# Kernel optimization log

Hardware: AMD Instinct MI355X
Metric: run time of the kernel (lower is better)

The kernel has to match this reference:

```python
import jax, jax.numpy as jnp
import numpy as np

HIDDEN = 4096
N_HEADS = 32
N_KV_HEADS = 8
HEAD_DIM = 128
MAX_POS = 4096
N_GROUPS = N_HEADS // N_KV_HEADS  # 4


def _sincos_table():
    # create_sinusoidal_positions(MAX_POS, HEAD_DIM) -> [MAX_POS, 1, 2*HEAD_DIM]
    inv_freq = 1.0 / 10000 ** (np.arange(0, HEAD_DIM, 2) / HEAD_DIM)
    freqs = np.einsum('i,j->ij', np.arange(MAX_POS), inv_freq).astype('float32')
    emb = np.concatenate((freqs, freqs), axis=-1)  # [MAX_POS, HEAD_DIM]
    out = np.concatenate((np.sin(emb)[:, None, :], np.cos(emb)[:, None, :]), axis=-1)
    return jnp.asarray(out[:, :, :MAX_POS])  # slice is a no-op since 2*HEAD_DIM < MAX_POS

_SINCOS = _sincos_table()


def _rotate_half(t):
    half = t.shape[-1] // 2
    return jnp.concatenate((-t[..., half:], t[..., :half]), axis=-1)


def setup_inputs() -> dict:
    key = jax.random.key(0)
    ks = jax.random.split(key, 9)
    B, S = 1, 2048
    scale = 0.02
    return {
        'hidden_states': jax.random.normal(ks[0], (B, S, HIDDEN), jnp.float32),
        'attention_mask': jnp.ones((B, 1, 1, S), jnp.bool_),
        'position_ids': jnp.broadcast_to(jnp.arange(S, dtype=jnp.int32)[None, :], (B, S)),
        'Wq': jax.random.normal(ks[1], (HIDDEN, N_HEADS * HEAD_DIM), jnp.float32) * scale,
        'bq': jnp.zeros((N_HEADS * HEAD_DIM,), jnp.float32),
        'Wk': jax.random.normal(ks[2], (HIDDEN, N_KV_HEADS * HEAD_DIM), jnp.float32) * scale,
        'bk': jnp.zeros((N_KV_HEADS * HEAD_DIM,), jnp.float32),
        'Wv': jax.random.normal(ks[3], (HIDDEN, N_KV_HEADS * HEAD_DIM), jnp.float32) * scale,
        'bv': jnp.zeros((N_KV_HEADS * HEAD_DIM,), jnp.float32),
        'Wo': jax.random.normal(ks[4], (N_HEADS * HEAD_DIM, HIDDEN), jnp.float32) * scale,
        'bo': jnp.zeros((HIDDEN,), jnp.float32),
    }


def reference(hidden_states, attention_mask, position_ids, Wq, bq, Wk, bk, Wv, bv, Wo, bo):
    B, S, _ = hidden_states.shape
    # QKV projections + split heads
    q = (hidden_states @ Wq + bq).reshape(B, S, N_HEADS, HEAD_DIM)
    k = (hidden_states @ Wk + bk).reshape(B, S, N_KV_HEADS, HEAD_DIM)
    v = (hidden_states @ Wv + bv).reshape(B, S, N_KV_HEADS, HEAD_DIM)
    # Rotary embedding: sincos[position_ids] -> [B,S,1,2*HEAD_DIM]
    sincos = _SINCOS[position_ids]
    sin_pos, cos_pos = jnp.split(sincos, 2, axis=-1)  # each [B,S,1,HEAD_DIM]
    k = k * cos_pos + _rotate_half(k) * sin_pos
    q = q * cos_pos + _rotate_half(q) * sin_pos
    # Causal mask combined with padding mask
    causal = jnp.tril(jnp.ones((S, S), jnp.bool_))[None, None]  # [1,1,S,S]
    mask = jnp.logical_and(attention_mask, causal)  # [B,1,S,S]
    # GQA: repeat kv heads
    k = jnp.repeat(k, N_GROUPS, axis=2)  # [B,S,H,D]
    v = jnp.repeat(v, N_GROUPS, axis=2)
    bias = jnp.where(mask, 0.0, jnp.finfo(jnp.float32).min).astype(jnp.float32)
    scores = jnp.einsum('bqhd,bkhd->bhqk', q, k) / jnp.sqrt(jnp.float32(HEAD_DIM)) + bias
    attn_weights = jax.nn.softmax(scores, axis=-1)  # [B,H,S,S]
    attn_output = jnp.einsum('bhqk,bkhd->bqhd', attn_weights, v).reshape(B, S, N_HEADS * HEAD_DIM)
    return attn_output @ Wo + bo
```

## Files before the change

### kernel.cpp

```cpp
#include <hip/hip_runtime.h>
#include <hip/hip_bf16.h>
#include <math.h>

typedef __bf16 bf16x8 __attribute__((ext_vector_type(8)));
typedef __bf16 bf16x4 __attribute__((ext_vector_type(4)));
typedef float  f32x4  __attribute__((ext_vector_type(4)));
typedef unsigned int u32;

#define S_LEN 2048
#define HID   4096
#define NH    32
#define NKV   8
#define HD    128

__device__ inline void gld_lds16(const __bf16* g, __bf16* l) {
  __builtin_amdgcn_global_load_lds((const __attribute__((address_space(1))) u32*)g,
                                   (__attribute__((address_space(3))) u32*)l,
                                   16, 0, 0);
}

__global__ void cast_bf16(const float* __restrict__ in, __bf16* __restrict__ out, int n4) {
  int i = blockIdx.x * blockDim.x + threadIdx.x;
  if (i < n4) {
    float4 v = ((const float4*)in)[i];
    bf16x4 o;
    o[0] = (__bf16)v.x; o[1] = (__bf16)v.y; o[2] = (__bf16)v.z; o[3] = (__bf16)v.w;
    ((bf16x4*)out)[i] = o;
  }
}

template <typename T>
__global__ void transpose_cast(const T* __restrict__ in, __bf16* __restrict__ out,
                               int ldi, int ldo) {
  __shared__ float tile[32][33];
  const int c0 = blockIdx.x * 32, r0 = blockIdx.y * 32;
  const int tx = threadIdx.x, ty = threadIdx.y;
  for (int j = 0; j < 32; j += 8)
    tile[ty + j][tx] = (float)in[(size_t)(r0 + ty + j) * ldi + c0 + tx];
  __syncthreads();
  for (int j = 0; j < 32; j += 8)
    out[(size_t)(c0 + ty + j) * ldo + r0 + tx] = (__bf16)tile[tx][ty + j];
}

__global__ void concat_bias(const float* __restrict__ bk, const float* __restrict__ bv,
                            float* __restrict__ out) {
  int i = blockIdx.x * blockDim.x + threadIdx.x;
  if (i < 2048) out[i] = (i < 1024) ? bk[i] : bv[i - 1024];
}

template <typename CT>
__global__ __launch_bounds__(256) void gemm_bt(const __bf16* __restrict__ A,
                                               const __bf16* __restrict__ Bt,
                                               const float* __restrict__ bias,
                                               CT* __restrict__ C,
                                               int M, int N, int K) {
  __shared__ __bf16 As[128 * 64];
  __shared__ __bf16 Bs[128 * 64];
  const int tid  = threadIdx.x;
  const int lane = tid & 63;
  const int lrow = lane & 15, quad = lane >> 4;
  const int wave = tid >> 6;
  const int wm = (wave & 1) * 64, wn = (wave >> 1) * 64;
  const int m0 = blockIdx.y * 128, n0 = blockIdx.x * 128;

  f32x4 acc[4][4] = {};

  const __bf16* aP[4];
  const __bf16* bP[4];
  __bf16* aL[4];
  __bf16* bL[4];
#pragma unroll
  for (int s = 0; s < 4; s++) {
    const int c = tid + 256 * s;
    const int row = c >> 3;
    const int kc = ((c & 7) + row) & 7;
    aP[s] = A + (size_t)(m0 + row) * K + kc * 8;
    bP[s] = Bt + (size_t)(n0 + row) * K + kc * 8;
    aL[s] = As + c * 8;
    bL[s] = Bs + c * 8;
  }

  int offA[2][4], offB[2][4];
#pragma unroll
  for (int h = 0; h < 2; h++)
#pragma unroll
    for (int t = 0; t < 4; t++) {
      const int ra = wm + t * 16 + lrow;
      const int rb = wn + t * 16 + lrow;
      offA[h][t] = (ra * 8 + ((h * 4 + quad - ra) & 7)) * 8;
      offB[h][t] = (rb * 8 + ((h * 4 + quad - rb) & 7)) * 8;
    }

  for (int k0 = 0; k0 < K; k0 += 64) {
    __syncthreads();
#pragma unroll
    for (int s = 0; s < 4; s++) {
      gld_lds16(aP[s] + k0, aL[s]);
      gld_lds16(bP[s] + k0, bL[s]);
    }
    __syncthreads();

#pragma unroll
    for (int h = 0; h < 2; h++) {
      bf16x8 af[4], bfr[4];
#pragma unroll
      for (int t = 0; t < 4; t++) {
        af[t]  = *(const bf16x8*)(As + offA[h][t]);
        bfr[t] = *(const bf16x8*)(Bs + offB[h][t]);
      }
#pragma unroll
      for (int i = 0; i < 4; i++)
#pragma unroll
        for (int j = 0; j < 4; j++)
          acc[i][j] = __builtin_amdgcn_mfma_f32_16x16x32_bf16(af[i], bfr[j], acc[i][j], 0, 0, 0);
    }
  }

#pragma unroll
  for (int i = 0; i < 4; i++) {
    const int row = m0 + wm + i * 16 + quad * 4;
#pragma unroll
    for (int j = 0; j < 4; j++) {
      const int col = n0 + wn + j * 16 + lrow;
      const float b = bias[col];
#pragma unroll
      for (int r = 0; r < 4; r++)
        C[(size_t)(row + r) * N + col] = (CT)(acc[i][j][r] + b);
    }
  }
}

__global__ void rope_inplace(__bf16* __restrict__ Q, __bf16* __restrict__ KV,
                             const int* __restrict__ pos_ids) {
  const int s = blockIdx.y;
  const int t = blockIdx.x * blockDim.x + threadIdx.x;
  const int h = t >> 6, j = t & 63;
  const float pos = (float)pos_ids[s];
  const float inv_freq = __builtin_exp2f((float)j * -0.2076205059304601f);
  const float ang = pos * inv_freq;
  float sn, cs;
  sincosf(ang, &sn, &cs);
  if (h < NH) {
    __bf16* p = Q + (size_t)s * HID + h * HD + j;
    const float x0 = (float)p[0], x1 = (float)p[64];
    p[0]  = (__bf16)(x0 * cs - x1 * sn);
    p[64] = (__bf16)(x1 * cs + x0 * sn);
  } else {
    const int hk = h - NH;
    __bf16* p = KV + (size_t)s * 2048 + hk * HD + j;
    const float x0 = (float)p[0], x1 = (float)p[64];
    p[0]  = (__bf16)(x0 * cs - x1 * sn);
    p[64] = (__bf16)(x1 * cs + x0 * sn);
  }
}

__global__ __launch_bounds__(256) void flash_attn(const __bf16* __restrict__ Qb,
                                                  const __bf16* __restrict__ Kb,
                                                  const __bf16* __restrict__ Vt,
                                                  __bf16* __restrict__ attn, int ldk) {
  __shared__ __bf16 Ks[2][32 * 128];
  __shared__ __bf16 Vs[2][128 * 32];
  __shared__ __bf16 Plds[4][2][16][40];
  const int tid  = threadIdx.x;
  const int wave = tid >> 6;
  const int lane = tid & 63;
  const int lrow = lane & 15, quad = lane >> 4;

  const int c = blockIdx.x & 255, p = blockIdx.x >> 8;
  const int h = c >> 3;
  const int xh = c & 7;
  const int xx = p ? xh : 15 - xh;
  const int bq0 = xx * 128;
  const int kvh = h >> 2;
  const int T0 = bq0 + wave * 16;
  const int T1 = T0 + 64;
  const int kend = bq0 + 128;

  const __bf16* kg[2];
  const __bf16* vg[2];
  __bf16* kL[2];
  __bf16* vL[2];
#pragma unroll
  for (int s = 0; s < 2; s++) {
    const int ck = tid + 256 * s;
    const int key = ck >> 4, kcb = ((ck & 15) + key) & 15;
    kg[s] = Kb + (size_t)key * ldk + kvh * HD + kcb * 8;
    kL[s] = (__bf16*)0 + ck * 8;
    const int cv = tid + 256 * s;
    const int d = cv >> 2, vcb = ((cv & 3) + d) & 3;
    vg[s] = Vt + (size_t)(kvh * HD + d) * S_LEN + vcb * 8;
    vL[s] = (__bf16*)0 + cv * 8;
  }

  int offK0[4], offK1[4], offV[8];
#pragma unroll
  for (int kc = 0; kc < 4; kc++) {
    const int rot = (kc * 4 + quad - lrow) & 15;
    offK0[kc] = (lrow * 16 + rot) * 8;
    offK1[kc] = ((lrow + 16) * 16 + rot) * 8;
  }
#pragma unroll
  for (int dt = 0; dt < 8; dt++) {
    const int d = dt * 16 + lrow;
    offV[dt] = (d * 4 + ((quad - d) & 3)) * 8;
  }

  bf16x8 qf[2][4];
#pragma unroll
  for (int m = 0; m < 2; m++) {
    const __bf16* qbase = Qb + (size_t)(T0 + m * 64 + lrow) * HID + h * HD + quad * 8;
#pragma unroll
    for (int kc = 0; kc < 4; kc++) qf[m][kc] = *(const bf16x8*)(qbase + kc * 32);
  }

  f32x4 o[2][8] = {};
  f32x4 lac[2] = {};
  bf16x8 ones;
#pragma unroll
  for (int j = 0; j < 8; j++) ones[j] = (__bf16)1.0f;

  const float cs = 0.08838834764831845f * 1.44269504088896f;

#pragma unroll
  for (int s = 0; s < 2; s++) {
    gld_lds16(kg[s], &Ks[0][0] + (size_t)(kL[s] - (__bf16*)0));
    gld_lds16(vg[s], &Vs[0][0] + (size_t)(vL[s] - (__bf16*)0));
  }

  int cur = 0;
  for (int kb = 0; kb < kend; kb += 32) {
    __syncthreads();
    if (kb + 32 < kend) {
      const int nxt = cur ^ 1;
#pragma unroll
      for (int s = 0; s < 2; s++) {
        gld_lds16(kg[s] + (size_t)(kb + 32) * ldk, &Ks[nxt][0] + (size_t)(kL[s] - (__bf16*)0));
        gld_lds16(vg[s] + (kb + 32), &Vs[nxt][0] + (size_t)(vL[s] - (__bf16*)0));
      }
    }

    bf16x8 kf0[4], kf1[4];
#pragma unroll
    for (int kc = 0; kc < 4; kc++) {
      kf0[kc] = *(const bf16x8*)(&Ks[cur][offK0[kc]]);
      kf1[kc] = *(const bf16x8*)(&Ks[cur][offK1[kc]]);
    }
    f32x4 s[2][2] = {};
#pragma unroll
    for (int kc = 0; kc < 4; kc++) {
      s[0][0] = __builtin_amdgcn_mfma_f32_16x16x32_bf16(qf[0][kc], kf0[kc], s[0][0], 0, 0, 0);
      s[0][1] = __builtin_amdgcn_mfma_f32_16x16x32_bf16(qf[0][kc], kf1[kc], s[0][1], 0, 0, 0);
      s[1][0] = __builtin_amdgcn_mfma_f32_16x16x32_bf16(qf[1][kc], kf0[kc], s[1][0], 0, 0, 0);
      s[1][1] = __builtin_amdgcn_mfma_f32_16x16x32_bf16(qf[1][kc], kf1[kc], s[1][1], 0, 0, 0);
    }
#pragma unroll
    for (int m = 0; m < 2; m++) {
      const int Tm = m ? T1 : T0;
#pragma unroll
      for (int n = 0; n < 2; n++) {
        const int col = kb + n * 16 + lrow;
#pragma unroll
        for (int r = 0; r < 4; r++) {
          const int row = Tm + quad * 4 + r;
          const float pv = (col <= row) ? __builtin_exp2f(s[m][n][r] * cs) : 0.0f;
          Plds[wave][m][quad * 4 + r][n * 16 + lrow] = (__bf16)pv;
        }
      }
    }
    bf16x8 pf0 = *(const bf16x8*)(&Plds[wave][0][lrow][quad * 8]);
    bf16x8 pf1 = *(const bf16x8*)(&Plds[wave][1][lrow][quad * 8]);
#pragma unroll
    for (int dt = 0; dt < 8; dt++) {
      bf16x8 vf = *(const bf16x8*)(&Vs[cur][offV[dt]]);
      o[0][dt] = __builtin_amdgcn_mfma_f32_16x16x32_bf16(pf0, vf, o[0][dt], 0, 0, 0);
      o[1][dt] = __builtin_amdgcn_mfma_f32_16x16x32_bf16(pf1, vf, o[1][dt], 0, 0, 0);
    }
    lac[0] = __builtin_amdgcn_mfma_f32_16x16x32_bf16(pf0, ones, lac[0], 0, 0, 0);
    lac[1] = __builtin_amdgcn_mfma_f32_16x16x32_bf16(pf1, ones, lac[1], 0, 0, 0);
    cur ^= 1;
  }

#pragma unroll
  for (int m = 0; m < 2; m++) {
    const int Tm = m ? T1 : T0;
#pragma unroll
    for (int r = 0; r < 4; r++) {
      const float inv_l = 1.0f / lac[m][r];
      const size_t rowoff = (size_t)(Tm + quad * 4 + r) * HID + h * HD;
#pragma unroll
      for (int dt = 0; dt < 8; dt++)
        attn[rowoff + dt * 16 + lrow] = (__bf16)(o[m][dt][r] * inv_l);
    }
  }
}

extern "C" void kernel_launch(void* const* d_in, const int* in_sizes, int n_in,
                              void* d_out, int out_size, void* d_ws, size_t ws_size,
                              hipStream_t stream) {
  const float* hs = (const float*)d_in[0];
  const int* pos = (const int*)d_in[2];
  const float* Wq = (const float*)d_in[3];
  const float* bq = (const float*)d_in[4];
  const float* Wk = (const float*)d_in[5];
  const float* bk = (const float*)d_in[6];
  const float* Wv = (const float*)d_in[7];
  const float* bv = (const float*)d_in[8];
  const float* Wo = (const float*)d_in[9];
  const float* bo = (const float*)d_in[10];
  float* out = (float*)d_out;
  char* ws = (char*)d_ws;
  char* oc = (char*)d_out;

  __bf16* bHS   = (__bf16*)(ws + 0);
  __bf16* bWT   = (__bf16*)(ws + ((size_t)16 << 20));
  __bf16* bAttn = bHS;
  __bf16* bQ   = (__bf16*)(oc + 0);
  __bf16* bKV  = (__bf16*)(oc + ((size_t)16 << 20));
  __bf16* bVt  = (__bf16*)(oc + ((size_t)24 << 20));
  float*  bKVb = (float*)(oc + ((size_t)28 << 20));

  dim3 tb(32, 8);

  cast_bf16<<<8192, 256, 0, stream>>>(hs, bHS, (S_LEN * HID) / 4);
  transpose_cast<float><<<dim3(128, 128), tb, 0, stream>>>(Wq, bWT, 4096, 4096);
  gemm_bt<__bf16><<<dim3(32, 16), 256, 0, stream>>>(bHS, bWT, bq, bQ, 2048, 4096, 4096);
  transpose_cast<float><<<dim3(32, 128), tb, 0, stream>>>(Wk, bWT, 1024, 4096);
  transpose_cast<float><<<dim3(32, 128), tb, 0, stream>>>(Wv, bWT + (size_t)1024 * 4096, 1024, 4096);
  concat_bias<<<8, 256, 0, stream>>>(bk, bv, bKVb);
  gemm_bt<__bf16><<<dim3(16, 16), 256, 0, stream>>>(bHS, bWT, bKVb, bKV, 2048, 2048, 4096);
  rope_inplace<<<dim3(10, 2048), 256, 0, stream>>>(bQ, bKV, pos);
  transpose_cast<__bf16><<<dim3(32, 64), tb, 0, stream>>>(bKV + 1024, bVt, 2048, 2048);
  flash_attn<<<512, 256, 0, stream>>>(bQ, bKV, bVt, bAttn, 2048);
  transpose_cast<float><<<dim3(128, 128), tb, 0, stream>>>(Wo, bWT, 4096, 4096);
  gemm_bt<float><<<dim3(32, 16), 256, 0, stream>>>(bAttn, bWT, bo, out, 2048, 4096, 4096);
}
```

Before: 567.9 us.

## Use 2-wave flash attention blocks with 64 query rows per wave and causal skipping

Flash attention now runs with 128 threads (2 waves) per block instead of 4, and each wave owns 64 contiguous query rows. Each K/V fragment read from LDS is therefore reused across four row tiles instead of two. Waves skip key blocks lying entirely above their causal diagonal, and tiles fully below the diagonal drop the per-element mask test. The costs are more registers per wave, fewer waves per block to hide latency, more loads per thread, and an adjusted V LDS swizzle.

```diff
diff --git a/kernel.cpp b/kernel.cpp
--- a/kernel.cpp
+++ b/kernel.cpp
@@ -154,13 +154,13 @@
   }
 }
 
-__global__ __launch_bounds__(256) void flash_attn(const __bf16* __restrict__ Qb,
-                                                  const __bf16* __restrict__ Kb,
-                                                  const __bf16* __restrict__ Vt,
-                                                  __bf16* __restrict__ attn, int ldk) {
+__global__ __launch_bounds__(128, 1) void flash_attn(const __bf16* __restrict__ Qb,
+                                                     const __bf16* __restrict__ Kb,
+                                                     const __bf16* __restrict__ Vt,
+                                                     __bf16* __restrict__ attn, int ldk) {
   __shared__ __bf16 Ks[2][32 * 128];
   __shared__ __bf16 Vs[2][128 * 32];
-  __shared__ __bf16 Plds[4][2][16][40];
+  __shared__ __bf16 Plds[2][4][16][40];
   const int tid  = threadIdx.x;
   const int wave = tid >> 6;
   const int lane = tid & 63;
@@ -172,24 +172,21 @@
   const int xx = p ? xh : 15 - xh;
   const int bq0 = xx * 128;
   const int kvh = h >> 2;
-  const int T0 = bq0 + wave * 16;
-  const int T1 = T0 + 64;
+  const int Tw = bq0 + wave * 64;
   const int kend = bq0 + 128;
 
-  const __bf16* kg[2];
-  const __bf16* vg[2];
-  __bf16* kL[2];
-  __bf16* vL[2];
-#pragma unroll
-  for (int s = 0; s < 2; s++) {
-    const int ck = tid + 256 * s;
+  const __bf16* kg[4];
+  const __bf16* vg[4];
+  int kL[4], vL[4];
+#pragma unroll
+  for (int s = 0; s < 4; s++) {
+    const int ck = tid + 128 * s;
     const int key = ck >> 4, kcb = ((ck & 15) + key) & 15;
     kg[s] = Kb + (size_t)key * ldk + kvh * HD + kcb * 8;
-    kL[s] = (__bf16*)0 + ck * 8;
-    const int cv = tid + 256 * s;
-    const int d = cv >> 2, vcb = ((cv & 3) + d) & 3;
+    kL[s] = ck * 8;
+    const int d = ck >> 2, vcb = ((ck & 3) - (d >> 1)) & 3;
     vg[s] = Vt + (size_t)(kvh * HD + d) * S_LEN + vcb * 8;
-    vL[s] = (__bf16*)0 + cv * 8;
+    vL[s] = ck * 8;
   }
 
   int offK0[4], offK1[4], offV[8];
@@ -202,19 +199,19 @@
 #pragma unroll
   for (int dt = 0; dt < 8; dt++) {
     const int d = dt * 16 + lrow;
-    offV[dt] = (d * 4 + ((quad - d) & 3)) * 8;
-  }
-
-  bf16x8 qf[2][4];
-#pragma unroll
-  for (int m = 0; m < 2; m++) {
-    const __bf16* qbase = Qb + (size_t)(T0 + m * 64 + lrow) * HID + h * HD + quad * 8;
+    offV[dt] = (d * 4 + ((quad + (d >> 1)) & 3)) * 8;
+  }
+
+  bf16x8 qf[4][4];
+#pragma unroll
+  for (int m = 0; m < 4; m++) {
+    const __bf16* qbase = Qb + (size_t)(Tw + m * 16 + lrow) * HID + h * HD + quad * 8;
 #pragma unroll
     for (int kc = 0; kc < 4; kc++) qf[m][kc] = *(const bf16x8*)(qbase + kc * 32);
   }
 
-  f32x4 o[2][8] = {};
-  f32x4 lac[2] = {};
+  f32x4 o[4][8] = {};
+  f32x4 lac[4] = {};
   bf16x8 ones;
 #pragma unroll
   for (int j = 0; j < 8; j++) ones[j] = (__bf16)1.0f;
@@ -222,9 +219,9 @@
   const float cs = 0.08838834764831845f * 1.44269504088896f;
 
 #pragma unroll
-  for (int s = 0; s < 2; s++) {
-    gld_lds16(kg[s], &Ks[0][0] + (size_t)(kL[s] - (__bf16*)0));
-    gld_lds16(vg[s], &Vs[0][0] + (size_t)(vL[s] - (__bf16*)0));
+  for (int s = 0; s < 4; s++) {
+    gld_lds16(kg[s], &Ks[0][0] + kL[s]);
+    gld_lds16(vg[s], &Vs[0][0] + vL[s]);
   }
 
   int cur = 0;
@@ -233,56 +230,71 @@
     if (kb + 32 < kend) {
       const int nxt = cur ^ 1;
 #pragma unroll
-      for (int s = 0; s < 2; s++) {
-        gld_lds16(kg[s] + (size_t)(kb + 32) * ldk, &Ks[nxt][0] + (size_t)(kL[s] - (__bf16*)0));
-        gld_lds16(vg[s] + (kb + 32), &Vs[nxt][0] + (size_t)(vL[s] - (__bf16*)0));
-      }
-    }
-
-    bf16x8 kf0[4], kf1[4];
-#pragma unroll
-    for (int kc = 0; kc < 4; kc++) {
-      kf0[kc] = *(const bf16x8*)(&Ks[cur][offK0[kc]]);
-      kf1[kc] = *(const bf16x8*)(&Ks[cur][offK1[kc]]);
-    }
-    f32x4 s[2][2] = {};
-#pragma unroll
-    for (int kc = 0; kc < 4; kc++) {
-      s[0][0] = __builtin_amdgcn_mfma_f32_16x16x32_bf16(qf[0][kc], kf0[kc], s[0][0], 0, 0, 0);
-      s[0][1] = __builtin_amdgcn_mfma_f32_16x16x32_bf16(qf[0][kc], kf1[kc], s[0][1], 0, 0, 0);
-      s[1][0] = __builtin_amdgcn_mfma_f32_16x16x32_bf16(qf[1][kc], kf0[kc], s[1][0], 0, 0, 0);
-      s[1][1] = __builtin_amdgcn_mfma_f32_16x16x32_bf16(qf[1][kc], kf1[kc], s[1][1], 0, 0, 0);
-    }
-#pragma unroll
-    for (int m = 0; m < 2; m++) {
-      const int Tm = m ? T1 : T0;
-#pragma unroll
-      for (int n = 0; n < 2; n++) {
-        const int col = kb + n * 16 + lrow;
-#pragma unroll
-        for (int r = 0; r < 4; r++) {
-          const int row = Tm + quad * 4 + r;
-          const float pv = (col <= row) ? __builtin_exp2f(s[m][n][r] * cs) : 0.0f;
-          Plds[wave][m][quad * 4 + r][n * 16 + lrow] = (__bf16)pv;
+      for (int s = 0; s < 4; s++) {
+        gld_lds16(kg[s] + (size_t)(kb + 32) * ldk, &Ks[nxt][0] + kL[s]);
+        gld_lds16(vg[s] + (kb + 32), &Vs[nxt][0] + vL[s]);
+      }
+    }
+
+    if (kb < Tw + 64) {
+      bf16x8 kf0[4], kf1[4];
+#pragma unroll
+      for (int kc = 0; kc < 4; kc++) {
+        kf0[kc] = *(const bf16x8*)(&Ks[cur][offK0[kc]]);
+        kf1[kc] = *(const bf16x8*)(&Ks[cur][offK1[kc]]);
+      }
+      f32x4 sc[4][2] = {};
+#pragma unroll
+      for (int kc = 0; kc < 4; kc++) {
+#pragma unroll
+        for (int m = 0; m < 4; m++) {
+          sc[m][0] = __builtin_amdgcn_mfma_f32_16x16x32_bf16(qf[m][kc], kf0[kc], sc[m][0], 0, 0, 0);
+          sc[m][1] = __builtin_amdgcn_mfma_f32_16x16x32_bf16(qf[m][kc], kf1[kc], sc[m][1], 0, 0, 0);
         }
       }
-    }
-    bf16x8 pf0 = *(const bf16x8*)(&Plds[wave][0][lrow][quad * 8]);
-    bf16x8 pf1 = *(const bf16x8*)(&Plds[wave][1][lrow][quad * 8]);
-#pragma unroll
-    for (int dt = 0; dt < 8; dt++) {
-      bf16x8 vf = *(const bf16x8*)(&Vs[cur][offV[dt]]);
-      o[0][dt] = __builtin_amdgcn_mfma_f32_16x16x32_bf16(pf0, vf, o[0][dt], 0, 0, 0);
-      o[1][dt] = __builtin_amdgcn_mfma_f32_16x16x32_bf16(pf1, vf, o[1][dt], 0, 0, 0);
-    }
-    lac[0] = __builtin_amdgcn_mfma_f32_16x16x32_bf16(pf0, ones, lac[0], 0, 0, 0);
-    lac[1] = __builtin_amdgcn_mfma_f32_16x16x32_bf16(pf1, ones, lac[1], 0, 0, 0);
+#pragma unroll
+      for (int m = 0; m < 4; m++) {
+        const int rmin = Tw + m * 16;
+        if (kb + 31 <= rmin) {
+#pragma unroll
+          for (int n = 0; n < 2; n++)
+#pragma unroll
+            for (int r = 0; r < 4; r++)
+              Plds[wave][m][quad * 4 + r][n * 16 + lrow] =
+                  (__bf16)__builtin_exp2f(sc[m][n][r] * cs);
+        } else {
+          const int rb = rmin + quad * 4;
+#pragma unroll
+          for (int n = 0; n < 2; n++) {
+            const int col = kb + n * 16 + lrow;
+#pragma unroll
+            for (int r = 0; r < 4; r++) {
+              const float pv = (col <= rb + r) ? __builtin_exp2f(sc[m][n][r] * cs) : 0.0f;
+              Plds[wave][m][quad * 4 + r][n * 16 + lrow] = (__bf16)pv;
+            }
+          }
+        }
+      }
+      bf16x8 pf[4];
+#pragma unroll
+      for (int m = 0; m < 4; m++) pf[m] = *(const bf16x8*)(&Plds[wave][m][lrow][quad * 8]);
+#pragma unroll
+      for (int dt = 0; dt < 8; dt++) {
+        bf16x8 vf = *(const bf16x8*)(&Vs[cur][offV[dt]]);
+#pragma unroll
+        for (int m = 0; m < 4; m++)
+          o[m][dt] = __builtin_amdgcn_mfma_f32_16x16x32_bf16(pf[m], vf, o[m][dt], 0, 0, 0);
+      }
+#pragma unroll
+      for (int m = 0; m < 4; m++)
+        lac[m] = __builtin_amdgcn_mfma_f32_16x16x32_bf16(pf[m], ones, lac[m], 0, 0, 0);
+    }
     cur ^= 1;
   }
 
 #pragma unroll
-  for (int m = 0; m < 2; m++) {
-    const int Tm = m ? T1 : T0;
+  for (int m = 0; m < 4; m++) {
+    const int Tm = Tw + m * 16;
 #pragma unroll
     for (int r = 0; r < 4; r++) {
       const float inv_l = 1.0f / lac[m][r];
@@ -330,7 +342,7 @@
   gemm_bt<__bf16><<<dim3(16, 16), 256, 0, stream>>>(bHS, bWT, bKVb, bKV, 2048, 2048, 4096);
   rope_inplace<<<dim3(10, 2048), 256, 0, stream>>>(bQ, bKV, pos);
   transpose_cast<__bf16><<<dim3(32, 64), tb, 0, stream>>>(bKV + 1024, bVt, 2048, 2048);
-  flash_attn<<<512, 256, 0, stream>>>(bQ, bKV, bVt, bAttn, 2048);
+  flash_attn<<<512, 128, 0, stream>>>(bQ, bKV, bVt, bAttn, 2048);
   transpose_cast<float><<<dim3(128, 128), tb, 0, stream>>>(Wo, bWT, 4096, 4096);
   gemm_bt<float><<<dim3(32, 16), 256, 0, stream>>>(bAttn, bWT, bo, out, 2048, 4096, 4096);
 }
```

Measured after the change: 621.7 us. 9.5% more time.

## Skip fully-masked causal tiles per wave, add unmasked fast path and swizzle fix

Applied to the files above, without the earlier changes.

Each wave now skips the QK^T and PV MFMAs for row groups whose rows all lie above the current key block, since those tiles are entirely masked. Tiles that are entirely below the diagonal skip the per-element causal compare. The V LDS swizzle changes to a new rotation, likely to cut bank conflicts on the transposed V reads, and s_setprio is raised around the MFMA bursts. The cost is added branching inside waves and a risk of imbalance across the block's waves, since the block barrier still forces them to step through every key block together.

```diff
diff --git a/kernel.cpp b/kernel.cpp
--- a/kernel.cpp
+++ b/kernel.cpp
@@ -178,18 +178,16 @@
 
   const __bf16* kg[2];
   const __bf16* vg[2];
-  __bf16* kL[2];
-  __bf16* vL[2];
+  int kL[2], vL[2];
 #pragma unroll
   for (int s = 0; s < 2; s++) {
     const int ck = tid + 256 * s;
     const int key = ck >> 4, kcb = ((ck & 15) + key) & 15;
     kg[s] = Kb + (size_t)key * ldk + kvh * HD + kcb * 8;
-    kL[s] = (__bf16*)0 + ck * 8;
-    const int cv = tid + 256 * s;
-    const int d = cv >> 2, vcb = ((cv & 3) + d) & 3;
+    kL[s] = ck * 8;
+    const int d = ck >> 2, vcb = ((ck & 3) - (d >> 1)) & 3;
     vg[s] = Vt + (size_t)(kvh * HD + d) * S_LEN + vcb * 8;
-    vL[s] = (__bf16*)0 + cv * 8;
+    vL[s] = ck * 8;
   }
 
   int offK0[4], offK1[4], offV[8];
@@ -202,7 +200,7 @@
 #pragma unroll
   for (int dt = 0; dt < 8; dt++) {
     const int d = dt * 16 + lrow;
-    offV[dt] = (d * 4 + ((quad - d) & 3)) * 8;
+    offV[dt] = (d * 4 + ((quad + (d >> 1)) & 3)) * 8;
   }
 
   bf16x8 qf[2][4];
@@ -223,8 +221,8 @@
 
 #pragma unroll
   for (int s = 0; s < 2; s++) {
-    gld_lds16(kg[s], &Ks[0][0] + (size_t)(kL[s] - (__bf16*)0));
-    gld_lds16(vg[s], &Vs[0][0] + (size_t)(vL[s] - (__bf16*)0));
+    gld_lds16(kg[s], &Ks[0][0] + kL[s]);
+    gld_lds16(vg[s], &Vs[0][0] + vL[s]);
   }
 
   int cur = 0;
@@ -234,49 +232,86 @@
       const int nxt = cur ^ 1;
 #pragma unroll
       for (int s = 0; s < 2; s++) {
-        gld_lds16(kg[s] + (size_t)(kb + 32) * ldk, &Ks[nxt][0] + (size_t)(kL[s] - (__bf16*)0));
-        gld_lds16(vg[s] + (kb + 32), &Vs[nxt][0] + (size_t)(vL[s] - (__bf16*)0));
-      }
-    }
-
-    bf16x8 kf0[4], kf1[4];
-#pragma unroll
-    for (int kc = 0; kc < 4; kc++) {
-      kf0[kc] = *(const bf16x8*)(&Ks[cur][offK0[kc]]);
-      kf1[kc] = *(const bf16x8*)(&Ks[cur][offK1[kc]]);
-    }
-    f32x4 s[2][2] = {};
-#pragma unroll
-    for (int kc = 0; kc < 4; kc++) {
-      s[0][0] = __builtin_amdgcn_mfma_f32_16x16x32_bf16(qf[0][kc], kf0[kc], s[0][0], 0, 0, 0);
-      s[0][1] = __builtin_amdgcn_mfma_f32_16x16x32_bf16(qf[0][kc], kf1[kc], s[0][1], 0, 0, 0);
-      s[1][0] = __builtin_amdgcn_mfma_f32_16x16x32_bf16(qf[1][kc], kf0[kc], s[1][0], 0, 0, 0);
-      s[1][1] = __builtin_amdgcn_mfma_f32_16x16x32_bf16(qf[1][kc], kf1[kc], s[1][1], 0, 0, 0);
-    }
-#pragma unroll
-    for (int m = 0; m < 2; m++) {
-      const int Tm = m ? T1 : T0;
-#pragma unroll
-      for (int n = 0; n < 2; n++) {
-        const int col = kb + n * 16 + lrow;
-#pragma unroll
-        for (int r = 0; r < 4; r++) {
-          const int row = Tm + quad * 4 + r;
-          const float pv = (col <= row) ? __builtin_exp2f(s[m][n][r] * cs) : 0.0f;
-          Plds[wave][m][quad * 4 + r][n * 16 + lrow] = (__bf16)pv;
-        }
-      }
-    }
-    bf16x8 pf0 = *(const bf16x8*)(&Plds[wave][0][lrow][quad * 8]);
-    bf16x8 pf1 = *(const bf16x8*)(&Plds[wave][1][lrow][quad * 8]);
-#pragma unroll
-    for (int dt = 0; dt < 8; dt++) {
-      bf16x8 vf = *(const bf16x8*)(&Vs[cur][offV[dt]]);
-      o[0][dt] = __builtin_amdgcn_mfma_f32_16x16x32_bf16(pf0, vf, o[0][dt], 0, 0, 0);
-      o[1][dt] = __builtin_amdgcn_mfma_f32_16x16x32_bf16(pf1, vf, o[1][dt], 0, 0, 0);
-    }
-    lac[0] = __builtin_amdgcn_mfma_f32_16x16x32_bf16(pf0, ones, lac[0], 0, 0, 0);
-    lac[1] = __builtin_amdgcn_mfma_f32_16x16x32_bf16(pf1, ones, lac[1], 0, 0, 0);
+        gld_lds16(kg[s] + (size_t)(kb + 32) * ldk, &Ks[nxt][0] + kL[s]);
+        gld_lds16(vg[s] + (kb + 32), &Vs[nxt][0] + vL[s]);
+      }
+    }
+
+    const bool live0 = (kb <= T0 + 15);
+    const bool live1 = (kb <= T1 + 15);
+
+    if (live1) {
+      bf16x8 kf0[4], kf1[4];
+#pragma unroll
+      for (int kc = 0; kc < 4; kc++) {
+        kf0[kc] = *(const bf16x8*)(&Ks[cur][offK0[kc]]);
+        kf1[kc] = *(const bf16x8*)(&Ks[cur][offK1[kc]]);
+      }
+      f32x4 sc[2][2] = {};
+      __builtin_amdgcn_s_setprio(1);
+      if (live0) {
+#pragma unroll
+        for (int kc = 0; kc < 4; kc++) {
+          sc[0][0] = __builtin_amdgcn_mfma_f32_16x16x32_bf16(qf[0][kc], kf0[kc], sc[0][0], 0, 0, 0);
+          sc[0][1] = __builtin_amdgcn_mfma_f32_16x16x32_bf16(qf[0][kc], kf1[kc], sc[0][1], 0, 0, 0);
+          sc[1][0] = __builtin_amdgcn_mfma_f32_16x16x32_bf16(qf[1][kc], kf0[kc], sc[1][0], 0, 0, 0);
+          sc[1][1] = __builtin_amdgcn_mfma_f32_16x16x32_bf16(qf[1][kc], kf1[kc], sc[1][1], 0, 0, 0);
+        }
+      } else {
+#pragma unroll
+        for (int kc = 0; kc < 4; kc++) {
+          sc[1][0] = __builtin_amdgcn_mfma_f32_16x16x32_bf16(qf[1][kc], kf0[kc], sc[1][0], 0, 0, 0);
+          sc[1][1] = __builtin_amdgcn_mfma_f32_16x16x32_bf16(qf[1][kc], kf1[kc], sc[1][1], 0, 0, 0);
+        }
+      }
+      __builtin_amdgcn_s_setprio(0);
+
+#pragma unroll
+      for (int m = 0; m < 2; m++) {
+        if (m == 0 && !live0) continue;
+        const int Tm = m ? T1 : T0;
+        if (kb + 31 <= Tm) {
+#pragma unroll
+          for (int n = 0; n < 2; n++)
+#pragma unroll
+            for (int r = 0; r < 4; r++)
+              Plds[wave][m][quad * 4 + r][n * 16 + lrow] =
+                  (__bf16)__builtin_exp2f(sc[m][n][r] * cs);
+        } else {
+          const int rb = Tm + quad * 4;
+#pragma unroll
+          for (int n = 0; n < 2; n++) {
+            const int col = kb + n * 16 + lrow;
+#pragma unroll
+            for (int r = 0; r < 4; r++) {
+              const float pv = (col <= rb + r) ? __builtin_exp2f(sc[m][n][r] * cs) : 0.0f;
+              Plds[wave][m][quad * 4 + r][n * 16 + lrow] = (__bf16)pv;
+            }
+          }
+        }
+      }
+      bf16x8 pf1 = *(const bf16x8*)(&Plds[wave][1][lrow][quad * 8]);
+      __builtin_amdgcn_s_setprio(1);
+      if (live0) {
+        bf16x8 pf0 = *(const bf16x8*)(&Plds[wave][0][lrow][quad * 8]);
+#pragma unroll
+        for (int dt = 0; dt < 8; dt++) {
+          bf16x8 vf = *(const bf16x8*)(&Vs[cur][offV[dt]]);
+          o[0][dt] = __builtin_amdgcn_mfma_f32_16x16x32_bf16(pf0, vf, o[0][dt], 0, 0, 0);
+          o[1][dt] = __builtin_amdgcn_mfma_f32_16x16x32_bf16(pf1, vf, o[1][dt], 0, 0, 0);
+        }
+        lac[0] = __builtin_amdgcn_mfma_f32_16x16x32_bf16(pf0, ones, lac[0], 0, 0, 0);
+        lac[1] = __builtin_amdgcn_mfma_f32_16x16x32_bf16(pf1, ones, lac[1], 0, 0, 0);
+      } else {
+#pragma unroll
+        for (int dt = 0; dt < 8; dt++) {
+          bf16x8 vf = *(const bf16x8*)(&Vs[cur][offV[dt]]);
+          o[1][dt] = __builtin_amdgcn_mfma_f32_16x16x32_bf16(pf1, vf, o[1][dt], 0, 0, 0);
+        }
+        lac[1] = __builtin_amdgcn_mfma_f32_16x16x32_bf16(pf1, ones, lac[1], 0, 0, 0);
+      }
+      __builtin_amdgcn_s_setprio(0);
+    }
     cur ^= 1;
   }
 
```

After: 575.6 us. No clear change (+1.4%).
